# Optimization experiments

Hardware: AMD Instinct MI355X
Metric: run time of the kernel (lower is better)

The kernel has to match this reference:

```python
import jax, jax.numpy as jnp
import numpy as np

# Device / mapping constants from the source (is_low_resistance=True branch)
V_REF = 0.25
G_MIN = 0.1
G_MAX = 1.0
K_V = 2.0 * V_REF  # x_to_V scale
N_AVG = 2.18
N_STD = 0.115


def setup_inputs() -> dict:
    key = jax.random.key(0)
    k_x, k_wp, k_wn, k_n = jax.random.split(key, 4)
    n_in, n_out, batch = 1024, 512, 128
    stdv = 1.0 / np.sqrt(n_in)
    x = jax.random.uniform(k_x, (batch, n_in), dtype=jnp.float32)
    w_pos = 0.5 + stdv * jax.random.normal(k_wp, (n_in, n_out), dtype=jnp.float32)
    w_neg = 0.5 + stdv * jax.random.normal(k_wn, (n_in, n_out), dtype=jnp.float32)
    b_pos = 0.5 * jnp.ones((n_out,), jnp.float32)
    b_neg = 0.5 * jnp.ones((n_out,), jnp.float32)
    # per-device I-V nonlinearity parameter n ~ N(n_avg, n_std), one per crossbar cell
    n_param = N_AVG + N_STD * jax.random.normal(k_n, (n_in + 1, 2 * n_out), dtype=jnp.float32)
    return {"x": x, "w_pos": w_pos, "w_neg": w_neg, "b_pos": b_pos, "b_neg": b_neg,
            "n_param": n_param}


def _memristor_dense(x, w_pos, w_neg, b_pos, b_neg, n_param):
    x = jnp.clip(x, 0.0, 1.0)
    # append bias rows, interleave pos/neg along output axis -> (n_in+1, 2*n_out)
    cw_pos = jnp.concatenate([w_pos, b_pos[None, :]], axis=0)
    cw_neg = jnp.concatenate([w_neg, b_neg[None, :]], axis=0)
    w = jnp.stack([cw_pos, cw_neg], axis=-1).reshape(cw_pos.shape[0], -1)
    # append ones column to inputs (bias voltage line)
    inp = jnp.concatenate([x, jnp.ones((x.shape[0], 1), x.dtype)], axis=1)  # (B, n_in+1)
    # weight -> effective conductance (differential scheme), then offset by G_min
    max_w = jnp.max(jnp.abs(w))
    k_G = (G_MAX - G_MIN) / max_w
    G = jnp.abs(k_G * w) + G_MIN  # (n_in+1, 2*n_out)
    # input -> voltage
    V = K_V * inp  # (B, n_in+1)
    # nonlinear-parameter I-V model: I = sign(V) * G * V_ref * (|V|/V_ref) ** (log2(n) + 1)
    # (satisfies n = I(2*V_ref) / (2 * I(V_ref)))
    exponent = jnp.log2(n_param) + 1.0  # (n_in+1, 2*n_out)
    v_ratio = jnp.abs(V) / V_REF  # (B, n_in+1)
    vr = v_ratio[:, :, None]  # (B, n_in+1, 1)
    vr_safe = jnp.where(vr > 0, vr, 1.0)
    pow_term = jnp.where(vr > 0, vr_safe ** exponent[None, :, :], 0.0)  # (B, n_in+1, 2*n_out)
    I_ind = jnp.sign(V)[:, :, None] * (G * V_REF)[None, :, :] * pow_term
    # sum currents along bit lines
    I = jnp.sum(I_ind, axis=1)  # (B, 2*n_out)
    # currents -> outputs (differential pairs are interleaved)
    y = (I[:, 0::2] - I[:, 1::2]) / (K_V * k_G)  # (B, n_out)
    return y


def reference(x, w_pos, w_neg, b_pos, b_neg, n_param):
    return _memristor_dense(x, w_pos, w_neg, b_pos, b_neg, n_param)
```

## Files before the change

kernel.cpp:

```cpp
#include <hip/hip_runtime.h>
#include <hip/hip_bf16.h>


#define LOG2F(v)  __builtin_amdgcn_logf(v)
#define EXP2F(v)  __builtin_amdgcn_exp2f(v)

#define NJ 16
#define NB 16
#define KI 64
#define KROW4 65
#define LROW 68

__global__ __launch_bounds__(256) void setup_kernel(
    const float* __restrict__ w_pos, const float* __restrict__ w_neg,
    const float* __restrict__ b_pos, const float* __restrict__ b_neg,
    float* __restrict__ y, int* __restrict__ ws) {
  const int t = threadIdx.x, blk = blockIdx.x;
  float4* y4 = (float4*)y;
  if (t < 64) y4[blk * 64 + t] = make_float4(0.f, 0.f, 0.f, 0.f);
  const float4* wp4 = (const float4*)w_pos;
  const float4* wn4 = (const float4*)w_neg;
  float m = 0.0f;
  #pragma unroll
  for (int r = 0; r < 2; ++r) {
    int i = blk * 512 + r * 256 + t;
    float4 a = wp4[i], b = wn4[i];
    m = fmaxf(m, fmaxf(fmaxf(fabsf(a.x), fabsf(a.y)), fmaxf(fabsf(a.z), fabsf(a.w))));
    m = fmaxf(m, fmaxf(fmaxf(fabsf(b.x), fabsf(b.y)), fmaxf(fabsf(b.z), fabsf(b.w))));
  }
  if (blk == 0) {
    m = fmaxf(m, fmaxf(fabsf(b_pos[t]), fabsf(b_pos[t + 256])));
    m = fmaxf(m, fmaxf(fabsf(b_neg[t]), fabsf(b_neg[t + 256])));
  }
  #pragma unroll
  for (int off = 32; off > 0; off >>= 1)
    m = fmaxf(m, __shfl_down(m, off, 64));
  __shared__ float sm[4];
  int lane = t & 63, wv = t >> 6;
  if (lane == 0) sm[wv] = m;
  __syncthreads();
  if (t == 0) {
    m = fmaxf(fmaxf(sm[0], sm[1]), fmaxf(sm[2], sm[3]));
    atomicMax(ws, __float_as_int(m));
  }
}

__global__ __launch_bounds__(256) void memristor_kernel(
    const float* __restrict__ x, const float* __restrict__ w_pos,
    const float* __restrict__ w_neg, const float* __restrict__ b_pos,
    const float* __restrict__ b_neg, const float* __restrict__ n_param,
    const float* __restrict__ ws, float* __restrict__ y) {
  __shared__ float4 sP[NJ * KROW4];
  __shared__ float  sL[NB * LROW];

  const float mw = __int_as_float(((const int*)ws)[0]);
  const float c0 = mw * (0.05f / 0.9f);

  const int j0 = blockIdx.x * NJ;
  const int b0 = blockIdx.y * NB;
  const int zt = blockIdx.z;
  const int t  = threadIdx.x;
  const int jj = t & 15;
  const int bb = t >> 4;
  float accP = 0.0f, accN = 0.0f;

  const float2* np2 = (const float2*)n_param;

  for (int c = 0; c < 2; ++c) {
    const int i0 = zt * 128 + c * KI;
    #pragma unroll
    for (int r = 0; r < (NB * KI) / 256; ++r) {
      int idx = r * 256 + t;
      int k  = idx & (KI - 1);
      int bl = idx >> 6;
      float v = x[(b0 + bl) * 1024 + i0 + k];
      v = fminf(fmaxf(v, 0.0f), 1.0f);
      sL[bl * LROW + k] = LOG2F(2.0f * v);
    }
    #pragma unroll
    for (int r = 0; r < (NJ * KI) / 256; ++r) {
      int idx = r * 256 + t;
      int jl = idx & (NJ - 1);
      int il = idx >> 4;
      int gi = i0 + il;
      float wp = w_pos[gi * 512 + j0 + jl];
      float wn = w_neg[gi * 512 + j0 + jl];
      float2 np = np2[gi * 512 + j0 + jl];
      sP[jl * KROW4 + il] = make_float4(
          fmaf(0.5f, fabsf(wp), c0), LOG2F(np.x) + 1.0f,
          fmaf(0.5f, fabsf(wn), c0), LOG2F(np.y) + 1.0f);
    }
    __syncthreads();
    const float4* pP = &sP[jj * KROW4];
    const float*  pL = &sL[bb * LROW];
    #pragma unroll 8
    for (int k = 0; k < KI; ++k) {
      float4 p = pP[k];
      float l  = pL[k];
      accP = fmaf(p.x, EXP2F(p.y * l), accP);
      accN = fmaf(p.z, EXP2F(p.w * l), accN);
    }
    __syncthreads();
  }

  if (zt == 7) {
    int jg = j0 + jj;
    float2 np = np2[1024 * 512 + jg];
    float a0 = fmaf(0.5f, fabsf(b_pos[jg]), c0);
    float a1 = fmaf(0.5f, fabsf(b_neg[jg]), c0);
    accP = fmaf(a0, EXP2F(LOG2F(np.x) + 1.0f), accP);
    accN = fmaf(a1, EXP2F(LOG2F(np.y) + 1.0f), accN);
  }

  atomicAdd(&y[(b0 + bb) * 512 + (j0 + jj)], accP - accN);
}

extern "C" void kernel_launch(void* const* d_in, const int* in_sizes, int n_in,
                              void* d_out, int out_size, void* d_ws, size_t ws_size,
                              hipStream_t stream) {
  const float* x       = (const float*)d_in[0];
  const float* w_pos   = (const float*)d_in[1];
  const float* w_neg   = (const float*)d_in[2];
  const float* b_pos   = (const float*)d_in[3];
  const float* b_neg   = (const float*)d_in[4];
  const float* n_param = (const float*)d_in[5];
  float* y   = (float*)d_out;

  setup_kernel<<<dim3(256), dim3(256), 0, stream>>>(
      w_pos, w_neg, b_pos, b_neg, y, (int*)d_ws);

  memristor_kernel<<<dim3(32, 8, 8), dim3(256), 0, stream>>>(
      x, w_pos, w_neg, b_pos, b_neg, n_param, (const float*)d_ws, y);
}
```

Baseline: 91.47 us.

## Register-block four batch rows per thread and widen split-K grid

Each thread now accumulates four batch rows instead of one, reusing each parameter float4 read from shared memory across four rows. The x log-values are stored transposed in LDS so one float4 load feeds those four rows. The split over K grows from 8 to 32 slices of 32, with 64 batch rows per block, which shortens each block's loop and changes the grid shape. The cost is four times as many output atomics per thread. Positive and negative terms are also folded into a single accumulator per row.

```diff
diff --git a/kernel.cpp b/kernel.cpp
--- a/kernel.cpp
+++ b/kernel.cpp
@@ -6,10 +6,9 @@
 #define EXP2F(v)  __builtin_amdgcn_exp2f(v)
 
 #define NJ 16
-#define NB 16
-#define KI 64
-#define KROW4 65
-#define LROW 68
+#define NB 64
+#define KI 32
+#define SLS4 17
 
 __global__ __launch_bounds__(256) void setup_kernel(
     const float* __restrict__ w_pos, const float* __restrict__ w_neg,
@@ -50,8 +49,8 @@
     const float* __restrict__ w_neg, const float* __restrict__ b_pos,
     const float* __restrict__ b_neg, const float* __restrict__ n_param,
     const float* __restrict__ ws, float* __restrict__ y) {
-  __shared__ float4 sP[NJ * KROW4];
-  __shared__ float  sL[NB * LROW];
+  __shared__ float4 sP[KI * NJ];
+  __shared__ float4 sL4[KI * SLS4];
 
   const float mw = __int_as_float(((const int*)ws)[0]);
   const float c0 = mw * (0.05f / 0.9f);
@@ -59,60 +58,70 @@
   const int j0 = blockIdx.x * NJ;
   const int b0 = blockIdx.y * NB;
   const int zt = blockIdx.z;
+  const int i0 = zt * KI;
   const int t  = threadIdx.x;
   const int jj = t & 15;
-  const int bb = t >> 4;
-  float accP = 0.0f, accN = 0.0f;
+  const int bq = t >> 4;
 
   const float2* np2 = (const float2*)n_param;
 
-  for (int c = 0; c < 2; ++c) {
-    const int i0 = zt * 128 + c * KI;
+  #pragma unroll
+  for (int r = 0; r < 2; ++r) {
+    int il = r * 16 + (t >> 4);
+    int jl = t & 15;
+    int gi = i0 + il;
+    float wp = w_pos[gi * 512 + j0 + jl];
+    float wn = w_neg[gi * 512 + j0 + jl];
+    float2 np = np2[gi * 512 + j0 + jl];
+    sP[il * NJ + jl] = make_float4(
+        fmaf(0.5f, fabsf(wp), c0), LOG2F(np.x) + 1.0f,
+        fmaf(0.5f, fabsf(wn), c0), LOG2F(np.y) + 1.0f);
+  }
+  {
+    float* sL = (float*)sL4;
+    const float4* x4 = (const float4*)x;
     #pragma unroll
-    for (int r = 0; r < (NB * KI) / 256; ++r) {
-      int idx = r * 256 + t;
-      int k  = idx & (KI - 1);
-      int bl = idx >> 6;
-      float v = x[(b0 + bl) * 1024 + i0 + k];
-      v = fminf(fmaxf(v, 0.0f), 1.0f);
-      sL[bl * LROW + k] = LOG2F(2.0f * v);
+    for (int r = 0; r < 2; ++r) {
+      int row = r * 32 + (t >> 3);
+      int k4  = t & 7;
+      float4 v = x4[(b0 + row) * 256 + zt * 8 + k4];
+      v.x = fminf(fmaxf(v.x, 0.0f), 1.0f);
+      v.y = fminf(fmaxf(v.y, 0.0f), 1.0f);
+      v.z = fminf(fmaxf(v.z, 0.0f), 1.0f);
+      v.w = fminf(fmaxf(v.w, 0.0f), 1.0f);
+      sL[(4 * k4 + 0) * (4 * SLS4) + row] = LOG2F(2.0f * v.x);
+      sL[(4 * k4 + 1) * (4 * SLS4) + row] = LOG2F(2.0f * v.y);
+      sL[(4 * k4 + 2) * (4 * SLS4) + row] = LOG2F(2.0f * v.z);
+      sL[(4 * k4 + 3) * (4 * SLS4) + row] = LOG2F(2.0f * v.w);
     }
-    #pragma unroll
-    for (int r = 0; r < (NJ * KI) / 256; ++r) {
-      int idx = r * 256 + t;
-      int jl = idx & (NJ - 1);
-      int il = idx >> 4;
-      int gi = i0 + il;
-      float wp = w_pos[gi * 512 + j0 + jl];
-      float wn = w_neg[gi * 512 + j0 + jl];
-      float2 np = np2[gi * 512 + j0 + jl];
-      sP[jl * KROW4 + il] = make_float4(
-          fmaf(0.5f, fabsf(wp), c0), LOG2F(np.x) + 1.0f,
-          fmaf(0.5f, fabsf(wn), c0), LOG2F(np.y) + 1.0f);
-    }
-    __syncthreads();
-    const float4* pP = &sP[jj * KROW4];
-    const float*  pL = &sL[bb * LROW];
-    #pragma unroll 8
-    for (int k = 0; k < KI; ++k) {
-      float4 p = pP[k];
-      float l  = pL[k];
-      accP = fmaf(p.x, EXP2F(p.y * l), accP);
-      accN = fmaf(p.z, EXP2F(p.w * l), accN);
-    }
-    __syncthreads();
+  }
+  __syncthreads();
+
+  float a0 = 0.0f, a1 = 0.0f, a2 = 0.0f, a3 = 0.0f;
+  #pragma unroll 4
+  for (int k = 0; k < KI; ++k) {
+    float4 p = sP[k * NJ + jj];
+    float4 l = sL4[k * SLS4 + bq];
+    a0 = fmaf(p.x, EXP2F(p.y * l.x), fmaf(-p.z, EXP2F(p.w * l.x), a0));
+    a1 = fmaf(p.x, EXP2F(p.y * l.y), fmaf(-p.z, EXP2F(p.w * l.y), a1));
+    a2 = fmaf(p.x, EXP2F(p.y * l.z), fmaf(-p.z, EXP2F(p.w * l.z), a2));
+    a3 = fmaf(p.x, EXP2F(p.y * l.w), fmaf(-p.z, EXP2F(p.w * l.w), a3));
   }
 
-  if (zt == 7) {
+  if (zt == 31) {
     int jg = j0 + jj;
     float2 np = np2[1024 * 512 + jg];
-    float a0 = fmaf(0.5f, fabsf(b_pos[jg]), c0);
-    float a1 = fmaf(0.5f, fabsf(b_neg[jg]), c0);
-    accP = fmaf(a0, EXP2F(LOG2F(np.x) + 1.0f), accP);
-    accN = fmaf(a1, EXP2F(LOG2F(np.y) + 1.0f), accN);
+    float p0 = fmaf(0.5f, fabsf(b_pos[jg]), c0);
+    float p1 = fmaf(0.5f, fabsf(b_neg[jg]), c0);
+    float bias = p0 * EXP2F(LOG2F(np.x) + 1.0f) - p1 * EXP2F(LOG2F(np.y) + 1.0f);
+    a0 += bias; a1 += bias; a2 += bias; a3 += bias;
   }
 
-  atomicAdd(&y[(b0 + bb) * 512 + (j0 + jj)], accP - accN);
+  const int row0 = b0 + 4 * bq;
+  atomicAdd(&y[(row0 + 0) * 512 + j0 + jj], a0);
+  atomicAdd(&y[(row0 + 1) * 512 + j0 + jj], a1);
+  atomicAdd(&y[(row0 + 2) * 512 + j0 + jj], a2);
+  atomicAdd(&y[(row0 + 3) * 512 + j0 + jj], a3);
 }
 
 extern "C" void kernel_launch(void* const* d_in, const int* in_sizes, int n_in,
@@ -129,6 +138,6 @@
   setup_kernel<<<dim3(256), dim3(256), 0, stream>>>(
       w_pos, w_neg, b_pos, b_neg, y, (int*)d_ws);
 
-  memristor_kernel<<<dim3(32, 8, 8), dim3(256), 0, stream>>>(
+  memristor_kernel<<<dim3(32, 2, 32), dim3(256), 0, stream>>>(
       x, w_pos, w_neg, b_pos, b_neg, n_param, (const float*)d_ws, y);
 }
```

Measured after the change: 87.58 us. 1.04x faster.
